# Kernel tuning notes

Measured on AMD Instinct MI355X. Metric: run time of the kernel, lower is better.

## Reference

```python
import jax, jax.numpy as jnp
import numpy as np

N = 50000
IN_DIM = 512
HID = 64
E = 800000


def setup_inputs() -> dict:
    key = jax.random.key(0)
    k1, k2, k3, k4 = jax.random.split(key, 4)
    x = jax.random.normal(k1, (N, IN_DIM), dtype=jnp.float32)
    edge_index = jax.random.randint(k2, (2, E), 0, N, dtype=jnp.int32)
    # Glorot-ish init for linear weights
    W1 = jax.random.normal(k3, (IN_DIM, HID), dtype=jnp.float32) / np.sqrt(IN_DIM)
    b1 = jnp.zeros((HID,), dtype=jnp.float32)
    W2 = jax.random.normal(k4, (HID, HID), dtype=jnp.float32) / np.sqrt(HID)
    b2 = jnp.zeros((HID,), dtype=jnp.float32)
    return {"x": x, "edge_index": edge_index, "W1": W1, "b1": b1, "W2": W2, "b2": b2}


def gcn_conv(x, src, dst, norm, W, b, n):
    # x' = D^{-1/2} (A+I) D^{-1/2} x W + b  (PyG GCNConv with self-loops)
    h = x @ W                                  # [N, out] dense GEMM
    msg = h[src] * norm[:, None]               # gather + scale per edge
    out = jax.ops.segment_sum(msg, dst, num_segments=n)  # scatter-add
    return out + b


def reference(x, edge_index, W1, b1, W2, b2):
    n = x.shape[0]
    loop = jnp.arange(n, dtype=edge_index.dtype)
    src = jnp.concatenate([edge_index[0], loop])  # add self-loops
    dst = jnp.concatenate([edge_index[1], loop])
    deg = jax.ops.segment_sum(jnp.ones_like(src, dtype=x.dtype), dst, num_segments=n)
    dinv = jnp.where(deg > 0, jax.lax.rsqrt(deg), 0.0)
    norm = dinv[src] * dinv[dst]               # symmetric normalization per edge
    h = gcn_conv(x, src, dst, norm, W1, b1, n)
    h = jax.nn.relu(h)
    # dropout is identity in eval mode (reference baseline)
    z = gcn_conv(h, src, dst, norm, W2, b2, n)
    return z
```

## Files before the change

kernel.cpp:

```cpp
#include <hip/hip_runtime.h>
#include <stdint.h>


typedef __attribute__((ext_vector_type(8))) short short8;
typedef __attribute__((ext_vector_type(4))) float f32x4;

#define SLOTS 64

__device__ __forceinline__ uint32_t bf16_rne(float f) {
  uint32_t u = __float_as_uint(f);
  return (u + 0x7FFFu + ((u >> 16) & 1u)) >> 16;
}

__global__ __launch_bounds__(256) void fill_kernel(const int* __restrict__ src,
                                                   const int* __restrict__ dst, int E,
                                                   int* __restrict__ cursor,
                                                   int* __restrict__ meta) {
  int i = blockIdx.x * 256 + threadIdx.x;
  if (i < E) {
    int s = src[i];
    int d = dst[i];
    int pos = atomicAdd(&cursor[d], 1);
    if (pos < SLOTS) meta[(size_t)d * SLOTS + pos] = s + 1;
  }
}

__global__ __launch_bounds__(256) void dinv_kernel(const int* __restrict__ cursor,
                                                   float* __restrict__ dinv, int n) {
  int i = blockIdx.x * 256 + threadIdx.x;
  if (i < n) dinv[i] = rsqrtf((float)(cursor[i] + 1));
}

__global__ __launch_bounds__(256) void wfrag_kernel(const float* __restrict__ W1,
                                                    const float* __restrict__ W2,
                                                    short8* __restrict__ wh1,
                                                    short8* __restrict__ wl1,
                                                    short8* __restrict__ wh2,
                                                    short8* __restrict__ wl2,
                                                    int K1, int K2) {
  int idx = blockIdx.x * 256 + threadIdx.x;
  int tot1 = (K1 >> 5) * 256;
  int tot2 = (K2 >> 5) * 256;
  const float* W;
  short8 *wh, *wl;
  if (idx < tot1) {
    W = W1; wh = wh1; wl = wl1;
  } else if (idx < tot1 + tot2) {
    idx -= tot1;
    W = W2; wh = wh2; wl = wl2;
  } else {
    return;
  }
  int lane = idx & 63;
  int ct = (idx >> 6) & 3;
  int kt = idx >> 8;
  int m = lane & 15, q = lane >> 4;
  int col = ct * 16 + m;
  short8 h, l;
#pragma unroll
  for (int j = 0; j < 8; ++j) {
    float f = W[(size_t)(kt * 32 + q * 8 + j) * 64 + col];
    uint32_t hb = bf16_rne(f);
    float hf = __uint_as_float(hb << 16);
    float lo = f - hf;
    h[j] = (short)hb;
    l[j] = (short)bf16_rne(lo);
  }
  wh[idx] = h;
  wl[idx] = l;
}

__global__ __launch_bounds__(256) void gemm_mfma_kernel(const float* __restrict__ A,
                                                        const short8* __restrict__ wh,
                                                        const short8* __restrict__ wl,
                                                        ushort* __restrict__ outb,
                                                        int n, int K) {
  const int t = threadIdx.x;
  const int lane = t & 63;
  const int m = lane & 15, q = lane >> 4;
  const int row0 = blockIdx.x * 128 + (t >> 6) * 32;
  int r0 = row0 + m;
  int r1 = row0 + 16 + m;
  if (r0 >= n) r0 = n - 1;
  if (r1 >= n) r1 = n - 1;
  const float* ap0 = A + (size_t)r0 * K + q * 8;
  const float* ap1 = A + (size_t)r1 * K + q * 8;
  const short8* whp = wh + lane;
  const short8* wlp = wl + lane;
  const int nkt = K >> 5;
  f32x4 acc[2][4];
#pragma unroll
  for (int g = 0; g < 2; ++g)
#pragma unroll
    for (int c = 0; c < 4; ++c) acc[g][c] = 0.f;

  float4 xa0 = *(const float4*)(ap0);
  float4 xa1 = *(const float4*)(ap0 + 4);
  float4 xb0 = *(const float4*)(ap1);
  float4 xb1 = *(const float4*)(ap1 + 4);
  short8 bh[4] = {whp[0], whp[64], whp[128], whp[192]};
  short8 bl[4] = {wlp[0], wlp[64], wlp[128], wlp[192]};

  auto cvt = [&](const float4& u0, const float4& u1, short8& hi, short8& lo) {
    float xf[8] = {u0.x, u0.y, u0.z, u0.w, u1.x, u1.y, u1.z, u1.w};
#pragma unroll
    for (int j = 0; j < 8; ++j) {
      uint32_t hb = bf16_rne(xf[j]);
      float hf = __uint_as_float(hb << 16);
      hi[j] = (short)hb;
      lo[j] = (short)bf16_rne(xf[j] - hf);
    }
  };
  auto compute = [&]() {
    short8 ah0, al0, ah1, al1;
    cvt(xa0, xa1, ah0, al0);
    cvt(xb0, xb1, ah1, al1);
#pragma unroll
    for (int c = 0; c < 4; ++c) {
      acc[0][c] = __builtin_amdgcn_mfma_f32_16x16x32_bf16(ah0, bh[c], acc[0][c], 0, 0, 0);
      acc[1][c] = __builtin_amdgcn_mfma_f32_16x16x32_bf16(ah1, bh[c], acc[1][c], 0, 0, 0);
    }
#pragma unroll
    for (int c = 0; c < 4; ++c) {
      acc[0][c] = __builtin_amdgcn_mfma_f32_16x16x32_bf16(ah0, bl[c], acc[0][c], 0, 0, 0);
      acc[1][c] = __builtin_amdgcn_mfma_f32_16x16x32_bf16(ah1, bl[c], acc[1][c], 0, 0, 0);
    }
#pragma unroll
    for (int c = 0; c < 4; ++c) {
      acc[0][c] = __builtin_amdgcn_mfma_f32_16x16x32_bf16(al0, bh[c], acc[0][c], 0, 0, 0);
      acc[1][c] = __builtin_amdgcn_mfma_f32_16x16x32_bf16(al1, bh[c], acc[1][c], 0, 0, 0);
    }
  };

  for (int kt = 0; kt < nkt - 1; ++kt) {
    const float* an0 = ap0 + 32;
    const float* an1 = ap1 + 32;
    float4 nxa0 = *(const float4*)(an0);
    float4 nxa1 = *(const float4*)(an0 + 4);
    float4 nxb0 = *(const float4*)(an1);
    float4 nxb1 = *(const float4*)(an1 + 4);
    const short8* whn = whp + 256;
    const short8* wln = wlp + 256;
    short8 nh[4] = {whn[0], whn[64], whn[128], whn[192]};
    short8 nl[4] = {wln[0], wln[64], wln[128], wln[192]};
    compute();
    xa0 = nxa0; xa1 = nxa1; xb0 = nxb0; xb1 = nxb1;
#pragma unroll
    for (int c = 0; c < 4; ++c) { bh[c] = nh[c]; bl[c] = nl[c]; }
    ap0 = an0; ap1 = an1; whp = whn; wlp = wln;
  }
  compute();

#pragma unroll
  for (int g = 0; g < 2; ++g)
#pragma unroll
    for (int i = 0; i < 4; ++i) {
      int rr = row0 + g * 16 + q * 4 + i;
      if (rr < n) {
        ushort* op = outb + (size_t)rr * 64 + m;
        op[0]  = (ushort)bf16_rne(acc[g][0][i]);
        op[16] = (ushort)bf16_rne(acc[g][1][i]);
        op[32] = (ushort)bf16_rne(acc[g][2][i]);
        op[48] = (ushort)bf16_rne(acc[g][3][i]);
      }
    }
}

__global__ __launch_bounds__(256) void agg_kernel(const ushort* __restrict__ H,
                                                  const int* __restrict__ deg,
                                                  const int* __restrict__ meta,
                                                  const float* __restrict__ dinv,
                                                  const float* __restrict__ bias,
                                                  float* __restrict__ out, int n, int do_relu) {
  const int t = threadIdx.x;
  const int sl = t & 7;
  const int v = blockIdx.x * 32 + (t >> 3);
  if (v >= n) return;
  const float dv = dinv[v];
  const float dvv = dv * dv;
  float acc[8];
  {
    uint4 hv = *(const uint4*)&H[(size_t)v * 64 + (sl << 3)];
    uint32_t u[4] = {hv.x, hv.y, hv.z, hv.w};
#pragma unroll
    for (int j = 0; j < 4; ++j) {
      acc[2 * j]     = __uint_as_float(u[j] << 16) * dvv;
      acc[2 * j + 1] = __uint_as_float(u[j] & 0xFFFF0000u) * dvv;
    }
  }
  int dg = deg[v];
  if (dg > SLOTS) dg = SLOTS;
  int nc = (dg + 7) >> 3;
  const int4* p = (const int4*)(meta + (size_t)v * SLOTS);

  int4 ma0, ma1, mb0, mb1;
  uint4 ra[8], rb[8];
  float wa[8], wb[8];
  auto gath = [&](int4 c0, int4 c1, uint4* r, float* wr) {
    int u[8] = {c0.x, c0.y, c0.z, c0.w, c1.x, c1.y, c1.z, c1.w};
#pragma unroll
    for (int j = 0; j < 8; ++j) {
      int idx = (u[j] > 0) ? (u[j] - 1) : 0;
      r[j] = *(const uint4*)&H[(size_t)idx * 64 + (sl << 3)];
      wr[j] = dinv[idx];
    }
  };
  auto consume = [&](int4 c0, int4 c1, const uint4* r, const float* wr) {
    int u[8] = {c0.x, c0.y, c0.z, c0.w, c1.x, c1.y, c1.z, c1.w};
#pragma unroll
    for (int j = 0; j < 8; ++j) {
      const float wgt = (u[j] > 0) ? wr[j] * dv : 0.f;
      uint32_t q[4] = {r[j].x, r[j].y, r[j].z, r[j].w};
#pragma unroll
      for (int k = 0; k < 4; ++k) {
        acc[2 * k]     = fmaf(__uint_as_float(q[k] << 16), wgt, acc[2 * k]);
        acc[2 * k + 1] = fmaf(__uint_as_float(q[k] & 0xFFFF0000u), wgt, acc[2 * k + 1]);
      }
    }
  };

  if (nc > 0) {
    ma0 = p[0]; ma1 = p[1];
    gath(ma0, ma1, ra, wa);
  }
  for (int c = 0; c < nc - 1; ++c) {
    mb0 = p[2 * c + 2]; mb1 = p[2 * c + 3];
    gath(mb0, mb1, rb, wb);
    consume(ma0, ma1, ra, wa);
    ma0 = mb0; ma1 = mb1;
#pragma unroll
    for (int j = 0; j < 8; ++j) { ra[j] = rb[j]; wa[j] = wb[j]; }
  }
  if (nc > 0) consume(ma0, ma1, ra, wa);

  const float4 blo = *(const float4*)&bias[sl << 3];
  const float4 bhi = *(const float4*)&bias[(sl << 3) + 4];
  float bb[8] = {blo.x, blo.y, blo.z, blo.w, bhi.x, bhi.y, bhi.z, bhi.w};
#pragma unroll
  for (int j = 0; j < 8; ++j) {
    acc[j] += bb[j];
    if (do_relu) acc[j] = fmaxf(acc[j], 0.f);
  }
  float* op = out + (size_t)v * 64 + (sl << 3);
  *(float4*)op = make_float4(acc[0], acc[1], acc[2], acc[3]);
  *(float4*)(op + 4) = make_float4(acc[4], acc[5], acc[6], acc[7]);
}

extern "C" void kernel_launch(void* const* d_in, const int* in_sizes, int n_in,
                              void* d_out, int out_size, void* d_ws, size_t ws_size,
                              hipStream_t stream) {
  const float* x = (const float*)d_in[0];
  const int* ei = (const int*)d_in[1];
  const float* W1 = (const float*)d_in[2];
  const float* b1 = (const float*)d_in[3];
  const float* W2 = (const float*)d_in[4];
  const float* b2 = (const float*)d_in[5];
  float* out = (float*)d_out;

  const int HID = in_sizes[3];
  const int IN_DIM = in_sizes[2] / HID;
  const int N = in_sizes[0] / IN_DIM;
  const int E = in_sizes[1] / 2;

  uint8_t* p = (uint8_t*)d_ws;
  auto alloc = [&](size_t bytes) {
    void* r = (void*)p;
    p += (bytes + 255) & ~(size_t)255;
    return r;
  };
  int* meta = (int*)alloc((size_t)N * SLOTS * 4);
  int* cursor = (int*)alloc((size_t)N * 4);
  float* dinv = (float*)alloc((size_t)N * 4);
  ushort* hb = (ushort*)alloc((size_t)N * HID * 2);
  float* h = (float*)alloc((size_t)N * HID * 4);
  short8* wh1 = (short8*)alloc((size_t)(IN_DIM >> 5) * 256 * 16);
  short8* wl1 = (short8*)alloc((size_t)(IN_DIM >> 5) * 256 * 16);
  short8* wh2 = (short8*)alloc((size_t)(HID >> 5) * 256 * 16);
  short8* wl2 = (short8*)alloc((size_t)(HID >> 5) * 256 * 16);

  const int* srcp = ei;
  const int* dstp = ei + E;

  const size_t zspan = (size_t)((uint8_t*)(cursor + N) - (uint8_t*)meta);
  hipMemsetAsync(meta, 0, zspan, stream);
  fill_kernel<<<(E + 255) / 256, 256, 0, stream>>>(srcp, dstp, E, cursor, meta);
  dinv_kernel<<<(N + 255) / 256, 256, 0, stream>>>(cursor, dinv, N);

  const int wtot = (IN_DIM >> 5) * 256 + (HID >> 5) * 256;
  wfrag_kernel<<<(wtot + 255) / 256, 256, 0, stream>>>(W1, W2, wh1, wl1, wh2, wl2,
                                                       IN_DIM, HID);

  gemm_mfma_kernel<<<(N + 127) / 128, 256, 0, stream>>>(x, wh1, wl1, hb, N, IN_DIM);
  agg_kernel<<<(N + 31) / 32, 256, 0, stream>>>(hb, cursor, meta, dinv, b1, h, N, 1);
  gemm_mfma_kernel<<<(N + 127) / 128, 256, 0, stream>>>(h, wh2, wl2, hb, N, HID);
  agg_kernel<<<(N + 31) / 32, 256, 0, stream>>>(hb, cursor, meta, dinv, b2, out, N, 0);
}
```

Measured before the change: 269.9 us.

## Store hidden activations as bf16, split GEMMs, inline dinv, shrink GEMM tiles

The layer-1 aggregation now writes the hidden activations in bf16 instead of fp32. A dedicated second GEMM consumes that bf16 input directly and runs two MFMA passes instead of three split passes. The dinv kernel is removed, and each aggregation recomputes rsqrt(deg+1) for the vertex and for every gathered neighbour. The first GEMM moves to 64-row blocks, one 16-row tile per wave, with a launch-bounds occupancy hint. Together these cut intermediate memory traffic and one kernel launch, at the cost of lower precision on the hidden layer and more per-edge rsqrt work.

```diff
diff --git a/kernel.cpp b/kernel.cpp
--- a/kernel.cpp
+++ b/kernel.cpp
@@ -23,12 +23,6 @@
     int pos = atomicAdd(&cursor[d], 1);
     if (pos < SLOTS) meta[(size_t)d * SLOTS + pos] = s + 1;
   }
-}
-
-__global__ __launch_bounds__(256) void dinv_kernel(const int* __restrict__ cursor,
-                                                   float* __restrict__ dinv, int n) {
-  int i = blockIdx.x * 256 + threadIdx.x;
-  if (i < n) dinv[i] = rsqrtf((float)(cursor[i] + 1));
 }
 
 __global__ __launch_bounds__(256) void wfrag_kernel(const float* __restrict__ W1,
@@ -70,113 +64,152 @@
   wl[idx] = l;
 }
 
-__global__ __launch_bounds__(256) void gemm_mfma_kernel(const float* __restrict__ A,
-                                                        const short8* __restrict__ wh,
-                                                        const short8* __restrict__ wl,
-                                                        ushort* __restrict__ outb,
-                                                        int n, int K) {
+__global__ __launch_bounds__(256, 4) void gemm1_kernel(const float* __restrict__ A,
+                                                       const short8* __restrict__ wh,
+                                                       const short8* __restrict__ wl,
+                                                       ushort* __restrict__ outb,
+                                                       int n, int K) {
   const int t = threadIdx.x;
   const int lane = t & 63;
   const int m = lane & 15, q = lane >> 4;
-  const int row0 = blockIdx.x * 128 + (t >> 6) * 32;
-  int r0 = row0 + m;
-  int r1 = row0 + 16 + m;
-  if (r0 >= n) r0 = n - 1;
-  if (r1 >= n) r1 = n - 1;
-  const float* ap0 = A + (size_t)r0 * K + q * 8;
-  const float* ap1 = A + (size_t)r1 * K + q * 8;
+  const int row0 = blockIdx.x * 64 + (t >> 6) * 16;
+  int r = row0 + m;
+  if (r >= n) r = n - 1;
+  const float* ap = A + (size_t)r * K + q * 8;
   const short8* whp = wh + lane;
   const short8* wlp = wl + lane;
   const int nkt = K >> 5;
-  f32x4 acc[2][4];
-#pragma unroll
-  for (int g = 0; g < 2; ++g)
-#pragma unroll
-    for (int c = 0; c < 4; ++c) acc[g][c] = 0.f;
-
-  float4 xa0 = *(const float4*)(ap0);
-  float4 xa1 = *(const float4*)(ap0 + 4);
-  float4 xb0 = *(const float4*)(ap1);
-  float4 xb1 = *(const float4*)(ap1 + 4);
+  f32x4 acc[4];
+#pragma unroll
+  for (int c = 0; c < 4; ++c) acc[c] = 0.f;
+
+  float4 x0 = *(const float4*)(ap);
+  float4 x1 = *(const float4*)(ap + 4);
   short8 bh[4] = {whp[0], whp[64], whp[128], whp[192]};
   short8 bl[4] = {wlp[0], wlp[64], wlp[128], wlp[192]};
 
-  auto cvt = [&](const float4& u0, const float4& u1, short8& hi, short8& lo) {
-    float xf[8] = {u0.x, u0.y, u0.z, u0.w, u1.x, u1.y, u1.z, u1.w};
+  auto compute = [&]() {
+    float xf[8] = {x0.x, x0.y, x0.z, x0.w, x1.x, x1.y, x1.z, x1.w};
+    short8 ah, al;
 #pragma unroll
     for (int j = 0; j < 8; ++j) {
       uint32_t hb = bf16_rne(xf[j]);
       float hf = __uint_as_float(hb << 16);
-      hi[j] = (short)hb;
-      lo[j] = (short)bf16_rne(xf[j] - hf);
-    }
+      ah[j] = (short)hb;
+      al[j] = (short)bf16_rne(xf[j] - hf);
+    }
+#pragma unroll
+    for (int c = 0; c < 4; ++c)
+      acc[c] = __builtin_amdgcn_mfma_f32_16x16x32_bf16(ah, bh[c], acc[c], 0, 0, 0);
+#pragma unroll
+    for (int c = 0; c < 4; ++c)
+      acc[c] = __builtin_amdgcn_mfma_f32_16x16x32_bf16(ah, bl[c], acc[c], 0, 0, 0);
+#pragma unroll
+    for (int c = 0; c < 4; ++c)
+      acc[c] = __builtin_amdgcn_mfma_f32_16x16x32_bf16(al, bh[c], acc[c], 0, 0, 0);
   };
-  auto compute = [&]() {
-    short8 ah0, al0, ah1, al1;
-    cvt(xa0, xa1, ah0, al0);
-    cvt(xb0, xb1, ah1, al1);
-#pragma unroll
-    for (int c = 0; c < 4; ++c) {
-      acc[0][c] = __builtin_amdgcn_mfma_f32_16x16x32_bf16(ah0, bh[c], acc[0][c], 0, 0, 0);
-      acc[1][c] = __builtin_amdgcn_mfma_f32_16x16x32_bf16(ah1, bh[c], acc[1][c], 0, 0, 0);
-    }
-#pragma unroll
-    for (int c = 0; c < 4; ++c) {
-      acc[0][c] = __builtin_amdgcn_mfma_f32_16x16x32_bf16(ah0, bl[c], acc[0][c], 0, 0, 0);
-      acc[1][c] = __builtin_amdgcn_mfma_f32_16x16x32_bf16(ah1, bl[c], acc[1][c], 0, 0, 0);
-    }
-#pragma unroll
-    for (int c = 0; c < 4; ++c) {
-      acc[0][c] = __builtin_amdgcn_mfma_f32_16x16x32_bf16(al0, bh[c], acc[0][c], 0, 0, 0);
-      acc[1][c] = __builtin_amdgcn_mfma_f32_16x16x32_bf16(al1, bh[c], acc[1][c], 0, 0, 0);
-    }
-  };
 
   for (int kt = 0; kt < nkt - 1; ++kt) {
-    const float* an0 = ap0 + 32;
-    const float* an1 = ap1 + 32;
-    float4 nxa0 = *(const float4*)(an0);
-    float4 nxa1 = *(const float4*)(an0 + 4);
-    float4 nxb0 = *(const float4*)(an1);
-    float4 nxb1 = *(const float4*)(an1 + 4);
+    const float* an = ap + 32;
+    float4 nx0 = *(const float4*)(an);
+    float4 nx1 = *(const float4*)(an + 4);
     const short8* whn = whp + 256;
     const short8* wln = wlp + 256;
     short8 nh[4] = {whn[0], whn[64], whn[128], whn[192]};
     short8 nl[4] = {wln[0], wln[64], wln[128], wln[192]};
     compute();
-    xa0 = nxa0; xa1 = nxa1; xb0 = nxb0; xb1 = nxb1;
+    x0 = nx0; x1 = nx1;
 #pragma unroll
     for (int c = 0; c < 4; ++c) { bh[c] = nh[c]; bl[c] = nl[c]; }
-    ap0 = an0; ap1 = an1; whp = whn; wlp = wln;
+    ap = an; whp = whn; wlp = wln;
   }
   compute();
 
 #pragma unroll
-  for (int g = 0; g < 2; ++g)
-#pragma unroll
-    for (int i = 0; i < 4; ++i) {
-      int rr = row0 + g * 16 + q * 4 + i;
-      if (rr < n) {
-        ushort* op = outb + (size_t)rr * 64 + m;
-        op[0]  = (ushort)bf16_rne(acc[g][0][i]);
-        op[16] = (ushort)bf16_rne(acc[g][1][i]);
-        op[32] = (ushort)bf16_rne(acc[g][2][i]);
-        op[48] = (ushort)bf16_rne(acc[g][3][i]);
-      }
-    }
+  for (int i = 0; i < 4; ++i) {
+    int rr = row0 + q * 4 + i;
+    if (rr < n) {
+      ushort* op = outb + (size_t)rr * 64 + m;
+      op[0]  = (ushort)bf16_rne(acc[0][i]);
+      op[16] = (ushort)bf16_rne(acc[1][i]);
+      op[32] = (ushort)bf16_rne(acc[2][i]);
+      op[48] = (ushort)bf16_rne(acc[3][i]);
+    }
+  }
+}
+
+__global__ __launch_bounds__(256, 4) void gemm2_kernel(const ushort* __restrict__ A,
+                                                       const short8* __restrict__ wh,
+                                                       const short8* __restrict__ wl,
+                                                       ushort* __restrict__ outb,
+                                                       int n, int K) {
+  const int t = threadIdx.x;
+  const int lane = t & 63;
+  const int m = lane & 15, q = lane >> 4;
+  const int row0 = blockIdx.x * 64 + (t >> 6) * 16;
+  int r = row0 + m;
+  if (r >= n) r = n - 1;
+  const ushort* ap = A + (size_t)r * K + q * 8;
+  const short8* whp = wh + lane;
+  const short8* wlp = wl + lane;
+  const int nkt = K >> 5;
+  f32x4 acc[4];
+#pragma unroll
+  for (int c = 0; c < 4; ++c) acc[c] = 0.f;
+
+  short8 ah = *(const short8*)(ap);
+  short8 bh[4] = {whp[0], whp[64], whp[128], whp[192]};
+  short8 bl[4] = {wlp[0], wlp[64], wlp[128], wlp[192]};
+
+  for (int kt = 0; kt < nkt; ++kt) {
+    short8 nah;
+    short8 nh[4], nl[4];
+    if (kt + 1 < nkt) {
+      nah = *(const short8*)(ap + 32);
+      const short8* whn = whp + 256;
+      const short8* wln = wlp + 256;
+#pragma unroll
+      for (int c = 0; c < 4; ++c) { nh[c] = whn[c * 64]; nl[c] = wln[c * 64]; }
+    }
+#pragma unroll
+    for (int c = 0; c < 4; ++c)
+      acc[c] = __builtin_amdgcn_mfma_f32_16x16x32_bf16(ah, bh[c], acc[c], 0, 0, 0);
+#pragma unroll
+    for (int c = 0; c < 4; ++c)
+      acc[c] = __builtin_amdgcn_mfma_f32_16x16x32_bf16(ah, bl[c], acc[c], 0, 0, 0);
+    if (kt + 1 < nkt) {
+      ah = nah;
+#pragma unroll
+      for (int c = 0; c < 4; ++c) { bh[c] = nh[c]; bl[c] = nl[c]; }
+      ap += 32; whp += 256; wlp += 256;
+    }
+  }
+
+#pragma unroll
+  for (int i = 0; i < 4; ++i) {
+    int rr = row0 + q * 4 + i;
+    if (rr < n) {
+      ushort* op = outb + (size_t)rr * 64 + m;
+      op[0]  = (ushort)bf16_rne(acc[0][i]);
+      op[16] = (ushort)bf16_rne(acc[1][i]);
+      op[32] = (ushort)bf16_rne(acc[2][i]);
+      op[48] = (ushort)bf16_rne(acc[3][i]);
+    }
+  }
 }
 
 __global__ __launch_bounds__(256) void agg_kernel(const ushort* __restrict__ H,
                                                   const int* __restrict__ deg,
                                                   const int* __restrict__ meta,
-                                                  const float* __restrict__ dinv,
                                                   const float* __restrict__ bias,
-                                                  float* __restrict__ out, int n, int do_relu) {
+                                                  float* __restrict__ outf,
+                                                  ushort* __restrict__ outb,
+                                                  int n, int do_relu) {
   const int t = threadIdx.x;
   const int sl = t & 7;
   const int v = blockIdx.x * 32 + (t >> 3);
   if (v >= n) return;
-  const float dv = dinv[v];
+  const float dv = rsqrtf((float)(deg[v] + 1));
   const float dvv = dv * dv;
   float acc[8];
   {
@@ -202,7 +235,7 @@
     for (int j = 0; j < 8; ++j) {
       int idx = (u[j] > 0) ? (u[j] - 1) : 0;
       r[j] = *(const uint4*)&H[(size_t)idx * 64 + (sl << 3)];
-      wr[j] = dinv[idx];
+      wr[j] = rsqrtf((float)(deg[idx] + 1));
     }
   };
   auto consume = [&](int4 c0, int4 c1, const uint4* r, const float* wr) {
@@ -237,13 +270,20 @@
   const float4 bhi = *(const float4*)&bias[(sl << 3) + 4];
   float bb[8] = {blo.x, blo.y, blo.z, blo.w, bhi.x, bhi.y, bhi.z, bhi.w};
 #pragma unroll
-  for (int j = 0; j < 8; ++j) {
-    acc[j] += bb[j];
-    if (do_relu) acc[j] = fmaxf(acc[j], 0.f);
-  }
-  float* op = out + (size_t)v * 64 + (sl << 3);
-  *(float4*)op = make_float4(acc[0], acc[1], acc[2], acc[3]);
-  *(float4*)(op + 4) = make_float4(acc[4], acc[5], acc[6], acc[7]);
+  for (int j = 0; j < 8; ++j) acc[j] += bb[j];
+  if (do_relu) {
+#pragma unroll
+    for (int j = 0; j < 8; ++j) acc[j] = fmaxf(acc[j], 0.f);
+    uint32_t w0 = bf16_rne(acc[0]) | (bf16_rne(acc[1]) << 16);
+    uint32_t w1 = bf16_rne(acc[2]) | (bf16_rne(acc[3]) << 16);
+    uint32_t w2 = bf16_rne(acc[4]) | (bf16_rne(acc[5]) << 16);
+    uint32_t w3 = bf16_rne(acc[6]) | (bf16_rne(acc[7]) << 16);
+    *(uint4*)&outb[(size_t)v * 64 + (sl << 3)] = make_uint4(w0, w1, w2, w3);
+  } else {
+    float* op = outf + (size_t)v * 64 + (sl << 3);
+    *(float4*)op = make_float4(acc[0], acc[1], acc[2], acc[3]);
+    *(float4*)(op + 4) = make_float4(acc[4], acc[5], acc[6], acc[7]);
+  }
 }
 
 extern "C" void kernel_launch(void* const* d_in, const int* in_sizes, int n_in,
@@ -270,9 +310,9 @@
   };
   int* meta = (int*)alloc((size_t)N * SLOTS * 4);
   int* cursor = (int*)alloc((size_t)N * 4);
-  float* dinv = (float*)alloc((size_t)N * 4);
-  ushort* hb = (ushort*)alloc((size_t)N * HID * 2);
-  float* h = (float*)alloc((size_t)N * HID * 4);
+  ushort* b1h = (ushort*)alloc((size_t)N * HID * 2);
+  ushort* b2h = (ushort*)alloc((size_t)N * HID * 2);
+  ushort* b3h = (ushort*)alloc((size_t)N * HID * 2);
   short8* wh1 = (short8*)alloc((size_t)(IN_DIM >> 5) * 256 * 16);
   short8* wl1 = (short8*)alloc((size_t)(IN_DIM >> 5) * 256 * 16);
   short8* wh2 = (short8*)alloc((size_t)(HID >> 5) * 256 * 16);
@@ -284,14 +324,13 @@
   const size_t zspan = (size_t)((uint8_t*)(cursor + N) - (uint8_t*)meta);
   hipMemsetAsync(meta, 0, zspan, stream);
   fill_kernel<<<(E + 255) / 256, 256, 0, stream>>>(srcp, dstp, E, cursor, meta);
-  dinv_kernel<<<(N + 255) / 256, 256, 0, stream>>>(cursor, dinv, N);
 
   const int wtot = (IN_DIM >> 5) * 256 + (HID >> 5) * 256;
   wfrag_kernel<<<(wtot + 255) / 256, 256, 0, stream>>>(W1, W2, wh1, wl1, wh2, wl2,
                                                        IN_DIM, HID);
 
-  gemm_mfma_kernel<<<(N + 127) / 128, 256, 0, stream>>>(x, wh1, wl1, hb, N, IN_DIM);
-  agg_kernel<<<(N + 31) / 32, 256, 0, stream>>>(hb, cursor, meta, dinv, b1, h, N, 1);
-  gemm_mfma_kernel<<<(N + 127) / 128, 256, 0, stream>>>(h, wh2, wl2, hb, N, HID);
-  agg_kernel<<<(N + 31) / 32, 256, 0, stream>>>(hb, cursor, meta, dinv, b2, out, N, 0);
-}
+  gemm1_kernel<<<(N + 63) / 64, 256, 0, stream>>>(x, wh1, wl1, b1h, N, IN_DIM);
+  agg_kernel<<<(N + 31) / 32, 256, 0, stream>>>(b1h, cursor, meta, b1, nullptr, b2h, N, 1);
+  gemm2_kernel<<<(N + 63) / 64, 256, 0, stream>>>(b2h, wh2, wl2, b3h, N, HID);
+  agg_kernel<<<(N + 31) / 32, 256, 0, stream>>>(b3h, cursor, meta, b2, out, nullptr, N, 0);
+}
```

Measured after the change: 279.5 us. 3.6% more time.
